# Performance work log

Measured on AMD Instinct MI355X. Metric: run time of the kernel, lower is better.

Reference implementation:

```python
import jax, jax.numpy as jnp
import numpy as np
from jax import lax

V, S, T, B = 32000, 64, 64, 64   # vocab, src_len, trg_len, batch
E, EH, DH = 128, 256, 256        # emb dim, enc hid, dec hid


def gru_cell(x, h, Wih, Whh, bih, bhh):
    # PyTorch GRU cell: gates ordered (r, z, n)
    gi = x @ Wih.T + bih
    gh = h @ Whh.T + bhh
    ir, iz, i_n = jnp.split(gi, 3, axis=-1)
    hr, hz, h_n = jnp.split(gh, 3, axis=-1)
    r = jax.nn.sigmoid(ir + hr)
    z = jax.nn.sigmoid(iz + hz)
    n = jnp.tanh(i_n + r * h_n)
    return (1.0 - z) * n + z * h


def setup_inputs() -> dict:
    key = jax.random.key(0)
    ks = iter(jax.random.split(key, 32))
    std = 0.01  # matches __init_weights(mean=0, std=0.01, const=0)
    def w(shape):
        return jax.random.normal(next(ks), shape, dtype=jnp.float32) * std
    return dict(
        src=jax.random.randint(next(ks), (S, B), 0, V),
        trg=jax.random.randint(next(ks), (T, B), 0, V),
        enc_emb=w((V, E)),
        enc_Wih_f=w((3 * EH, E)), enc_Whh_f=w((3 * EH, EH)),
        enc_bih_f=jnp.zeros((3 * EH,), jnp.float32), enc_bhh_f=jnp.zeros((3 * EH,), jnp.float32),
        enc_Wih_b=w((3 * EH, E)), enc_Whh_b=w((3 * EH, EH)),
        enc_bih_b=jnp.zeros((3 * EH,), jnp.float32), enc_bhh_b=jnp.zeros((3 * EH,), jnp.float32),
        enc_fc_W=w((DH, 2 * EH)), enc_fc_b=jnp.zeros((DH,), jnp.float32),
        attn_W=w((DH, 2 * EH + DH)), attn_b=jnp.zeros((DH,), jnp.float32),
        attn_v=w((1, DH)),
        dec_emb=w((V, E)),
        dec_Wih=w((3 * DH, 2 * EH + E)), dec_Whh=w((3 * DH, DH)),
        dec_bih=jnp.zeros((3 * DH,), jnp.float32), dec_bhh=jnp.zeros((3 * DH,), jnp.float32),
        fc_W=w((V, 2 * EH + DH + E)), fc_b=jnp.zeros((V,), jnp.float32),
    )


def reference(src, trg, enc_emb, enc_Wih_f, enc_Whh_f, enc_bih_f, enc_bhh_f,
              enc_Wih_b, enc_Whh_b, enc_bih_b, enc_bhh_b, enc_fc_W, enc_fc_b,
              attn_W, attn_b, attn_v, dec_emb, dec_Wih, dec_Whh, dec_bih,
              dec_bhh, fc_W, fc_b):
    # ---- Encoder: bidirectional GRU (dropout in eval mode => identity) ----
    emb = enc_emb[src]  # [S, B, E]
    h0 = jnp.zeros((src.shape[1], EH), emb.dtype)

    def step_f(h, x):
        h2 = gru_cell(x, h, enc_Wih_f, enc_Whh_f, enc_bih_f, enc_bhh_f)
        return h2, h2

    def step_b(h, x):
        h2 = gru_cell(x, h, enc_Wih_b, enc_Whh_b, enc_bih_b, enc_bhh_b)
        return h2, h2

    h_f, outs_f = lax.scan(step_f, h0, emb)
    h_b, outs_b_rev = lax.scan(step_b, h0, emb[::-1])
    enc_outs = jnp.concatenate([outs_f, outs_b_rev[::-1]], axis=-1)  # [S, B, 2*EH]
    hidden = jnp.tanh(jnp.concatenate([h_f, h_b], axis=-1) @ enc_fc_W.T + enc_fc_b)  # [B, DH]

    # ---- Decoder: per-step Bahdanau attention + GRU (teacher forcing) ----
    enc_bse = enc_outs.transpose(1, 0, 2)            # [B, S, 2*EH]
    W_h = attn_W[:, :DH]                             # hidden part of attn linear
    W_e = attn_W[:, DH:]                             # encoder part
    enc_proj = jnp.einsum('bse,he->bsh', enc_bse, W_e) + attn_b  # precomputed [B, S, DH]
    v = attn_v[0]                                    # [DH]

    def dec_step(h, tok):
        embd = dec_emb[tok]                                         # [B, E]
        energy = jnp.tanh(enc_proj + (h @ W_h.T)[:, None, :])       # [B, S, DH]
        scores = jnp.einsum('bsh,h->bs', energy, v)                 # [B, S]
        a = jax.nn.softmax(scores, axis=1)
        weighted = jnp.einsum('bs,bse->be', a, enc_bse)             # [B, 2*EH]
        x = jnp.concatenate([embd, weighted], axis=-1)              # [B, E+2*EH]
        h2 = gru_cell(x, h, dec_Wih, dec_Whh, dec_bih, dec_bhh)     # [B, DH]
        pred = jnp.concatenate([h2, weighted, embd], axis=-1) @ fc_W.T + fc_b  # [B, V]
        return h2, pred

    _, preds = lax.scan(dec_step, hidden, trg[:-1])                 # [T-1, B, V]
    outputs = jnp.concatenate(
        [jnp.zeros((1, preds.shape[1], preds.shape[2]), preds.dtype), preds], axis=0)
    return outputs
```

## Files before the change

kernel.cpp:

```cpp
#include <hip/hip_runtime.h>
#include <math.h>


__device__ __forceinline__ float sigmoidf_(float x) { return 1.0f / (1.0f + expf(-x)); }

typedef __attribute__((ext_vector_type(8))) short bf16x8;
typedef __attribute__((ext_vector_type(4))) float f32x4;
typedef __attribute__((ext_vector_type(8))) unsigned short ushort8;

__device__ __forceinline__ unsigned short f2bf(float f) {
  unsigned u = __float_as_uint(f);
  unsigned r = (u + 0x7fffu + ((u >> 16) & 1u)) >> 16;
  return (unsigned short)r;
}

__global__ __launch_bounds__(256) void k_zero(float* __restrict__ p, int n4) {
  int i = blockIdx.x * 256 + threadIdx.x;
  if (i < n4) ((float4*)p)[i] = make_float4(0.f, 0.f, 0.f, 0.f);
}

__global__ __launch_bounds__(256) void k_cvt_bf16(const float* __restrict__ in,
                                                  unsigned short* __restrict__ out, int n8) {
  int i = blockIdx.x * 256 + threadIdx.x;
  int stride = gridDim.x * 256;
  for (; i < n8; i += stride) {
    float4 a = ((const float4*)in)[2 * i];
    float4 b = ((const float4*)in)[2 * i + 1];
    ushort8 v;
    v[0] = f2bf(a.x); v[1] = f2bf(a.y); v[2] = f2bf(a.z); v[3] = f2bf(a.w);
    v[4] = f2bf(b.x); v[5] = f2bf(b.y); v[6] = f2bf(b.z); v[7] = f2bf(b.w);
    ((ushort8*)out)[i] = v;
  }
}

__global__ __launch_bounds__(256) void k_gather(const float* __restrict__ tab,
                                                const int* __restrict__ idx,
                                                float* __restrict__ out, int rows) {
  int g = blockIdx.x * 256 + threadIdx.x;
  int row = g >> 5, c = g & 31;
  if (row < rows) {
    int tok = idx[row];
    ((float4*)(out + (size_t)row * 128))[c] = ((const float4*)(tab + (size_t)tok * 128))[c];
  }
}

__global__ __launch_bounds__(256) void k_gemm_nt(const float* __restrict__ A, int lda,
                                                 const float* __restrict__ Bm, int ldb,
                                                 const float* __restrict__ bias,
                                                 float* __restrict__ C, int ldc, int K) {
  __shared__ float As[16][68];
  __shared__ float Bs[16][68];
  int tid = threadIdx.x;
  int m0 = blockIdx.y * 64, n0 = blockIdx.x * 64;
  int lm = tid >> 2, lk = (tid & 3) * 4;
  int tm = (tid >> 4) * 4, tn = (tid & 15) * 4;
  float acc[4][4] = {};
  for (int k0 = 0; k0 < K; k0 += 16) {
    float4 av = *(const float4*)(A + (size_t)(m0 + lm) * lda + k0 + lk);
    float4 bv = *(const float4*)(Bm + (size_t)(n0 + lm) * ldb + k0 + lk);
    __syncthreads();
    As[lk + 0][lm] = av.x; As[lk + 1][lm] = av.y; As[lk + 2][lm] = av.z; As[lk + 3][lm] = av.w;
    Bs[lk + 0][lm] = bv.x; Bs[lk + 1][lm] = bv.y; Bs[lk + 2][lm] = bv.z; Bs[lk + 3][lm] = bv.w;
    __syncthreads();
#pragma unroll
    for (int k = 0; k < 16; k++) {
      float4 a4 = *(const float4*)&As[k][tm];
      float4 b4 = *(const float4*)&Bs[k][tn];
      float ar[4] = {a4.x, a4.y, a4.z, a4.w};
      float br[4] = {b4.x, b4.y, b4.z, b4.w};
#pragma unroll
      for (int i = 0; i < 4; i++)
#pragma unroll
        for (int j = 0; j < 4; j++) acc[i][j] += ar[i] * br[j];
    }
  }
  float4 bb = *(const float4*)(bias + n0 + tn);
  float br[4] = {bb.x, bb.y, bb.z, bb.w};
#pragma unroll
  for (int i = 0; i < 4; i++) {
    float* crow = C + (size_t)(m0 + tm + i) * ldc + n0 + tn;
    *(float4*)crow = make_float4(acc[i][0] + br[0], acc[i][1] + br[1],
                                 acc[i][2] + br[2], acc[i][3] + br[3]);
  }
}

__global__ __launch_bounds__(256) void k_enc_step(
    const float* __restrict__ gi_f, const float* __restrict__ gi_b,
    const float* __restrict__ Whh_f, const float* __restrict__ Whh_b,
    const float* __restrict__ bhh_f, const float* __restrict__ bhh_b,
    const float* __restrict__ hinf, const float* __restrict__ hinb,
    float* __restrict__ houtf, float* __restrict__ houtb,
    float* __restrict__ enc_bse, int t) {
  int blk = blockIdx.x;
  int dir = blk >> 6;
  int jt = (blk >> 3) & 7, bg = blk & 7;
  const float* gi  = dir ? gi_b  : gi_f;
  const float* Whh = dir ? Whh_b : Whh_f;
  const float* bhh = dir ? bhh_b : bhh_f;
  const float* hin = dir ? hinb  : hinf;
  float* hout      = dir ? houtb : houtf;
  int s = dir ? (63 - t) : t;
  int tid = threadIdx.x;
  int b_l = tid & 7, j_l = tid >> 3;
  int b = bg * 8 + b_l, j = jt * 32 + j_l;
  __shared__ float hs[8][260];
  for (int i = tid; i < 2048; i += 256)
    hs[i >> 8][i & 255] = hin[(bg * 8 + (i >> 8)) * 256 + (i & 255)];
  __syncthreads();
  const float4* wr = (const float4*)(Whh + (size_t)j * 256);
  const float4* wz = (const float4*)(Whh + (size_t)(256 + j) * 256);
  const float4* wn = (const float4*)(Whh + (size_t)(512 + j) * 256);
  const float4* hv = (const float4*)&hs[b_l][0];
  float hr = 0.f, hz = 0.f, hn = 0.f;
#pragma unroll 8
  for (int k = 0; k < 64; k++) {
    float4 h4 = hv[k];
    float4 r4 = wr[k], z4 = wz[k], n4 = wn[k];
    hr += h4.x * r4.x + h4.y * r4.y + h4.z * r4.z + h4.w * r4.w;
    hz += h4.x * z4.x + h4.y * z4.y + h4.z * z4.z + h4.w * z4.w;
    hn += h4.x * n4.x + h4.y * n4.y + h4.z * n4.z + h4.w * n4.w;
  }
  hr += bhh[j]; hz += bhh[256 + j]; hn += bhh[512 + j];
  size_t gib = (size_t)(s * 64 + b) * 768;
  float r = sigmoidf_(gi[gib + j] + hr);
  float z = sigmoidf_(gi[gib + 256 + j] + hz);
  float n = tanhf(gi[gib + 512 + j] + r * hn);
  float h2 = (1.f - z) * n + z * hs[b_l][j];
  hout[b * 256 + j] = h2;
  enc_bse[((size_t)b * 64 + s) * 512 + dir * 256 + j] = h2;
}

__global__ __launch_bounds__(256) void k_hidden(const float* __restrict__ hf,
                                                const float* __restrict__ hb,
                                                const float* __restrict__ W,
                                                const float* __restrict__ bias,
                                                float* __restrict__ hdec) {
  int b = blockIdx.x, j = threadIdx.x;
  __shared__ float cat[512];
  cat[j] = hf[b * 256 + j];
  cat[256 + j] = hb[b * 256 + j];
  __syncthreads();
  const float4* wrow = (const float4*)(W + (size_t)j * 512);
  const float4* cv = (const float4*)cat;
  float acc = 0.f;
#pragma unroll 8
  for (int k = 0; k < 128; k++) {
    float4 w4 = wrow[k], c4 = cv[k];
    acc += w4.x * c4.x + w4.y * c4.y + w4.z * c4.z + w4.w * c4.w;
  }
  hdec[b * 256 + j] = tanhf(acc + bias[j]);
}

__global__ __launch_bounds__(256) void k_attn(
    const float* __restrict__ hdec, const float* __restrict__ attn_W,
    const float* __restrict__ attn_v, const float* __restrict__ enc_proj,
    const float* __restrict__ enc_bse, const float* __restrict__ embd_all,
    float* __restrict__ weighted, float* __restrict__ Z, int t) {
  int b = blockIdx.x, tid = threadIdx.x;
  __shared__ float hs[256], hW[256], vs[256], sc[64];
  hs[tid] = hdec[b * 256 + tid];
  vs[tid] = attn_v[tid];
  __syncthreads();
  {
    const float4* wrow = (const float4*)(attn_W + (size_t)tid * 768);
    const float4* hv = (const float4*)hs;
    float acc = 0.f;
#pragma unroll 8
    for (int k = 0; k < 64; k++) {
      float4 w4 = wrow[k], h4 = hv[k];
      acc += w4.x * h4.x + w4.y * h4.y + w4.z * h4.z + w4.w * h4.w;
    }
    hW[tid] = acc;
  }
  __syncthreads();
  int w = tid >> 6, l = tid & 63;
  for (int s = w; s < 64; s += 4) {
    const float* ep = enc_proj + ((size_t)b * 64 + s) * 256;
    float p = 0.f;
#pragma unroll
    for (int i = 0; i < 4; i++) {
      int h = l + i * 64;
      p += vs[h] * tanhf(ep[h] + hW[h]);
    }
#pragma unroll
    for (int o = 32; o > 0; o >>= 1) p += __shfl_xor(p, o, 64);
    if (l == 0) sc[s] = p;
  }
  __syncthreads();
  if (tid < 64) {
    float x = sc[tid], m = x;
#pragma unroll
    for (int o = 32; o > 0; o >>= 1) m = fmaxf(m, __shfl_xor(m, o, 64));
    float e = expf(x - m), ssum = e;
#pragma unroll
    for (int o = 32; o > 0; o >>= 1) ssum += __shfl_xor(ssum, o, 64);
    sc[tid] = e / ssum;
  }
  __syncthreads();
  float a0 = 0.f, a1 = 0.f;
  const float* eb = enc_bse + (size_t)b * 64 * 512;
  for (int s = 0; s < 64; s++) {
    float a = sc[s];
    a0 += a * eb[s * 512 + tid];
    a1 += a * eb[s * 512 + 256 + tid];
  }
  size_t zr = (size_t)(t * 64 + b) * 896;
  weighted[b * 512 + tid] = a0;
  weighted[b * 512 + 256 + tid] = a1;
  Z[zr + 256 + tid] = a0;
  Z[zr + 512 + tid] = a1;
  if (tid < 128) Z[zr + 768 + tid] = embd_all[(size_t)(t * 64 + b) * 128 + tid];
}

__global__ __launch_bounds__(256) void k_dec_gru(
    const float* __restrict__ weighted, const float* __restrict__ gi_emb,
    const float* __restrict__ Wih, const float* __restrict__ Whh,
    const float* __restrict__ bhh, const float* __restrict__ hin,
    float* __restrict__ hout, float* __restrict__ Z, int t) {
  int blk = blockIdx.x;
  int jt = blk & 7, bg = blk >> 3;
  int tid = threadIdx.x;
  int b_l = tid & 7, j_l = tid >> 3;
  int b = bg * 8 + b_l, j = jt * 32 + j_l;
  __shared__ float ws2[8][516];
  __shared__ float hs[8][260];
  for (int i = tid; i < 4096; i += 256)
    ws2[i >> 9][i & 511] = weighted[(bg * 8 + (i >> 9)) * 512 + (i & 511)];
  for (int i = tid; i < 2048; i += 256)
    hs[i >> 8][i & 255] = hin[(bg * 8 + (i >> 8)) * 256 + (i & 255)];
  __syncthreads();
  float gr = 0.f, gz = 0.f, gn = 0.f;
  {
    const float4* wr = (const float4*)(Wih + (size_t)j * 640 + 128);
    const float4* wz = (const float4*)(Wih + (size_t)(256 + j) * 640 + 128);
    const float4* wn = (const float4*)(Wih + (size_t)(512 + j) * 640 + 128);
    const float4* xv = (const float4*)&ws2[b_l][0];
#pragma unroll 8
    for (int k = 0; k < 128; k++) {
      float4 x4 = xv[k];
      float4 r4 = wr[k], z4 = wz[k], n4 = wn[k];
      gr += x4.x * r4.x + x4.y * r4.y + x4.z * r4.z + x4.w * r4.w;
      gz += x4.x * z4.x + x4.y * z4.y + x4.z * z4.z + x4.w * z4.w;
      gn += x4.x * n4.x + x4.y * n4.y + x4.z * n4.z + x4.w * n4.w;
    }
  }
  float hr = bhh[j], hz = bhh[256 + j], hn = bhh[512 + j];
  {
    const float4* ur = (const float4*)(Whh + (size_t)j * 256);
    const float4* uz = (const float4*)(Whh + (size_t)(256 + j) * 256);
    const float4* un = (const float4*)(Whh + (size_t)(512 + j) * 256);
    const float4* hv = (const float4*)&hs[b_l][0];
#pragma unroll 8
    for (int k = 0; k < 64; k++) {
      float4 h4 = hv[k];
      float4 r4 = ur[k], z4 = uz[k], n4 = un[k];
      hr += h4.x * r4.x + h4.y * r4.y + h4.z * r4.z + h4.w * r4.w;
      hz += h4.x * z4.x + h4.y * z4.y + h4.z * z4.z + h4.w * z4.w;
      hn += h4.x * n4.x + h4.y * n4.y + h4.z * n4.z + h4.w * n4.w;
    }
  }
  size_t gib = (size_t)(t * 64 + b) * 768;
  float r = sigmoidf_(gi_emb[gib + j] + gr + hr);
  float z = sigmoidf_(gi_emb[gib + 256 + j] + gz + hz);
  float n = tanhf(gi_emb[gib + 512 + j] + gn + r * hn);
  float h2 = (1.f - z) * n + z * hs[b_l][j];
  hout[b * 256 + j] = h2;
  Z[(size_t)(t * 64 + b) * 896 + j] = h2;
}

__global__ __launch_bounds__(256) void k_fc_mfma(const unsigned short* __restrict__ Zb16,
                                                 const unsigned short* __restrict__ Wb16,
                                                 const float* __restrict__ bias,
                                                 float* __restrict__ out) {
  __shared__ unsigned short As[128 * 64];
  __shared__ unsigned short Bs[128 * 64];
  int tid = threadIdx.x;
  int l = tid & 63, w = tid >> 6;
  int m0 = blockIdx.y * 128, n0 = blockIdx.x * 128;
  int wr = w >> 1, wc = w & 1;
  f32x4 acc[4][4] = {};

  int lrow = l >> 3;
  int lk = (l & 7) * 8;

  for (int k0 = 0; k0 < 896; k0 += 64) {
    __syncthreads();
#pragma unroll
    for (int i = 0; i < 4; i++) {
      int c = i * 4 + w;
      const unsigned short* ga = Zb16 + (size_t)(m0 + c * 8 + lrow) * 896 + k0 + lk;
      const unsigned short* gb = Wb16 + (size_t)(n0 + c * 8 + lrow) * 896 + k0 + lk;
      __builtin_amdgcn_global_load_lds((const __attribute__((address_space(1))) void*)ga,
                                       (__attribute__((address_space(3))) void*)&As[c * 512],
                                       16, 0, 0);
      __builtin_amdgcn_global_load_lds((const __attribute__((address_space(1))) void*)gb,
                                       (__attribute__((address_space(3))) void*)&Bs[c * 512],
                                       16, 0, 0);
    }
    __syncthreads();
#pragma unroll
    for (int ks = 0; ks < 2; ks++) {
      bf16x8 aF[4], bF[4];
#pragma unroll
      for (int i = 0; i < 4; i++)
        aF[i] = *(const bf16x8*)&As[(wr * 64 + i * 16 + (l & 15)) * 64 + ks * 32 + (l >> 4) * 8];
#pragma unroll
      for (int j = 0; j < 4; j++)
        bF[j] = *(const bf16x8*)&Bs[(wc * 64 + j * 16 + (l & 15)) * 64 + ks * 32 + (l >> 4) * 8];
#pragma unroll
      for (int i = 0; i < 4; i++)
#pragma unroll
        for (int j = 0; j < 4; j++)
          acc[i][j] = __builtin_amdgcn_mfma_f32_16x16x32_bf16(aF[i], bF[j], acc[i][j], 0, 0, 0);
    }
  }
  int cl = l & 15, rg = l >> 4;
#pragma unroll
  for (int j = 0; j < 4; j++) {
    int n = n0 + wc * 64 + j * 16 + cl;
    float bb = bias[n];
#pragma unroll
    for (int i = 0; i < 4; i++) {
      int mb = m0 + wr * 64 + i * 16 + rg * 4;
#pragma unroll
      for (int r = 0; r < 4; r++) {
        int m = mb + r;
        if (m < 4032) out[(size_t)(m + 64) * 32000 + n] = acc[i][j][r] + bb;
      }
    }
  }
}

extern "C" void kernel_launch(void* const* d_in, const int* in_sizes, int n_in,
                              void* d_out, int out_size, void* d_ws, size_t ws_size,
                              hipStream_t stream) {
  const int* src = (const int*)d_in[0];
  const int* trg = (const int*)d_in[1];
  const float* enc_emb = (const float*)d_in[2];
  const float* eWih_f  = (const float*)d_in[3];
  const float* eWhh_f  = (const float*)d_in[4];
  const float* ebih_f  = (const float*)d_in[5];
  const float* ebhh_f  = (const float*)d_in[6];
  const float* eWih_b  = (const float*)d_in[7];
  const float* eWhh_b  = (const float*)d_in[8];
  const float* ebih_b  = (const float*)d_in[9];
  const float* ebhh_b  = (const float*)d_in[10];
  const float* efc_W   = (const float*)d_in[11];
  const float* efc_b   = (const float*)d_in[12];
  const float* attn_W  = (const float*)d_in[13];
  const float* attn_b  = (const float*)d_in[14];
  const float* attn_v  = (const float*)d_in[15];
  const float* dec_emb = (const float*)d_in[16];
  const float* dWih    = (const float*)d_in[17];
  const float* dWhh    = (const float*)d_in[18];
  const float* dbih    = (const float*)d_in[19];
  const float* dbhh    = (const float*)d_in[20];
  const float* fc_W    = (const float*)d_in[21];
  const float* fc_b    = (const float*)d_in[22];
  float* out = (float*)d_out;
  float* ws = (float*)d_ws;

  size_t o = 0;
  float* emb_src  = ws + o; o += (size_t)4096 * 128;
  float* embd_all = ws + o; o += (size_t)4032 * 128;
  float* gi_f     = ws + o; o += (size_t)4096 * 768;
  float* gi_b     = ws + o; o += (size_t)4096 * 768;
  float* gi_emb   = ws + o; o += (size_t)4032 * 768;
  float* enc_bse  = ws + o; o += (size_t)4096 * 512;
  float* enc_proj = ws + o; o += (size_t)4096 * 256;
  float* h_f0 = ws + o; o += 16384;
  float* h_b0 = ws + o; o += 16384;
  float* h_f1 = ws + o; o += 16384;
  float* h_b1 = ws + o; o += 16384;
  float* h_d0 = ws + o; o += 16384;
  float* h_d1 = ws + o; o += 16384;
  float* wt   = ws + o; o += 64 * 512;
  float* Zb   = ws + o; o += (size_t)4096 * 896;
  unsigned short* Zb16 = (unsigned short*)(ws + o); o += (size_t)4096 * 896 / 2;
  unsigned short* Wb16 = (unsigned short*)(ws + o); o += (size_t)32000 * 896 / 2;

  k_zero<<<2000, 256, 0, stream>>>(out, 512000);
  k_zero<<<32, 256, 0, stream>>>(h_f0, 8192);
  k_zero<<<56, 256, 0, stream>>>(Zb + (size_t)4032 * 896, 14336);
  k_gather<<<512, 256, 0, stream>>>(enc_emb, src, emb_src, 4096);
  k_gather<<<504, 256, 0, stream>>>(dec_emb, trg, embd_all, 4032);

  k_cvt_bf16<<<2048, 256, 0, stream>>>(fc_W, Wb16, 3584000);

  k_gemm_nt<<<dim3(12, 64), 256, 0, stream>>>(emb_src, 128, eWih_f, 128, ebih_f, gi_f, 768, 128);
  k_gemm_nt<<<dim3(12, 64), 256, 0, stream>>>(emb_src, 128, eWih_b, 128, ebih_b, gi_b, 768, 128);
  k_gemm_nt<<<dim3(12, 63), 256, 0, stream>>>(embd_all, 128, dWih, 640, dbih, gi_emb, 768, 128);

  for (int t = 0; t < 64; t++) {
    const float* hif = (t & 1) ? h_f1 : h_f0;
    const float* hib = (t & 1) ? h_b1 : h_b0;
    float* hof = (t & 1) ? h_f0 : h_f1;
    float* hob = (t & 1) ? h_b0 : h_b1;
    k_enc_step<<<128, 256, 0, stream>>>(gi_f, gi_b, eWhh_f, eWhh_b, ebhh_f, ebhh_b,
                                        hif, hib, hof, hob, enc_bse, t);
  }
  k_hidden<<<64, 256, 0, stream>>>(h_f0, h_b0, efc_W, efc_b, h_d0);
  k_gemm_nt<<<dim3(4, 64), 256, 0, stream>>>(enc_bse, 512, attn_W + 256, 768, attn_b,
                                             enc_proj, 256, 512);

  for (int t = 0; t < 63; t++) {
    const float* hi = (t & 1) ? h_d1 : h_d0;
    float* ho = (t & 1) ? h_d0 : h_d1;
    k_attn<<<64, 256, 0, stream>>>(hi, attn_W, attn_v, enc_proj, enc_bse, embd_all, wt, Zb, t);
    k_dec_gru<<<64, 256, 0, stream>>>(wt, gi_emb, dWih, dWhh, dbhh, hi, ho, Zb, t);
  }

  k_cvt_bf16<<<1024, 256, 0, stream>>>(Zb, Zb16, 458752);
  k_fc_mfma<<<dim3(250, 32), 256, 0, stream>>>(Zb16, Wb16, fc_b, out);
}
```

Baseline: 5.204 ms.

## Fuse encoder and decoder time loops into persistent scan kernels, precompute attention-input projection

Replaces the 64 per-step encoder launches and the 126 per-step decoder launches with one persistent kernel each, with one block per (direction, batch) or per batch keeping the hidden state in shared memory across steps. Uses linearity to precompute enc_bse·Wih_ctx (PRE) once with a bf16 MFMA GEMM, so each decoder step only needs an attention-weighted sum of PRE rows instead of a 512-wide matvec. The enc_proj GEMM also moves to bf16 MFMA, which adds rounding error. In exchange, each recurrent step now runs on only 64–128 blocks, each serially streaming its weights.

```diff
diff --git a/kernel.cpp b/kernel.cpp
--- a/kernel.cpp
+++ b/kernel.cpp
@@ -33,6 +33,24 @@
   }
 }
 
+__global__ __launch_bounds__(256) void k_cvt_slice(const float* __restrict__ in,
+                                                   unsigned short* __restrict__ out,
+                                                   int rows, int ld, int col0, int cols) {
+  int g = blockIdx.x * 256 + threadIdx.x;
+  int c8 = cols >> 3;
+  int n8 = rows * c8;
+  if (g < n8) {
+    int r = g / c8, c = g % c8;
+    const float* p = in + (size_t)r * ld + col0 + c * 8;
+    float4 a = ((const float4*)p)[0];
+    float4 b = ((const float4*)p)[1];
+    ushort8 v;
+    v[0] = f2bf(a.x); v[1] = f2bf(a.y); v[2] = f2bf(a.z); v[3] = f2bf(a.w);
+    v[4] = f2bf(b.x); v[5] = f2bf(b.y); v[6] = f2bf(b.z); v[7] = f2bf(b.w);
+    ((ushort8*)(out + (size_t)r * cols + c * 8))[0] = v;
+  }
+}
+
 __global__ __launch_bounds__(256) void k_gather(const float* __restrict__ tab,
                                                 const int* __restrict__ idx,
                                                 float* __restrict__ out, int rows) {
@@ -42,6 +60,14 @@
     int tok = idx[row];
     ((float4*)(out + (size_t)row * 128))[c] = ((const float4*)(tab + (size_t)tok * 128))[c];
   }
+}
+
+__global__ __launch_bounds__(256) void k_embZ(const float* __restrict__ emb,
+                                              float* __restrict__ Z) {
+  int g = blockIdx.x * 256 + threadIdx.x;
+  int row = g >> 5, c = g & 31;
+  if (row < 4032)
+    ((float4*)(Z + (size_t)row * 896 + 768))[c] = ((const float4*)(emb + (size_t)row * 128))[c];
 }
 
 __global__ __launch_bounds__(256) void k_gemm_nt(const float* __restrict__ A, int lda,
@@ -84,50 +110,49 @@
   }
 }
 
-__global__ __launch_bounds__(256) void k_enc_step(
+__global__ __launch_bounds__(256) void k_enc_scan(
     const float* __restrict__ gi_f, const float* __restrict__ gi_b,
     const float* __restrict__ Whh_f, const float* __restrict__ Whh_b,
     const float* __restrict__ bhh_f, const float* __restrict__ bhh_b,
-    const float* __restrict__ hinf, const float* __restrict__ hinb,
-    float* __restrict__ houtf, float* __restrict__ houtb,
-    float* __restrict__ enc_bse, int t) {
+    float* __restrict__ hf_out, float* __restrict__ hb_out,
+    float* __restrict__ enc_bse) {
   int blk = blockIdx.x;
-  int dir = blk >> 6;
-  int jt = (blk >> 3) & 7, bg = blk & 7;
+  int dir = blk >> 6, b = blk & 63;
+  int j = threadIdx.x;
   const float* gi  = dir ? gi_b  : gi_f;
   const float* Whh = dir ? Whh_b : Whh_f;
   const float* bhh = dir ? bhh_b : bhh_f;
-  const float* hin = dir ? hinb  : hinf;
-  float* hout      = dir ? houtb : houtf;
-  int s = dir ? (63 - t) : t;
-  int tid = threadIdx.x;
-  int b_l = tid & 7, j_l = tid >> 3;
-  int b = bg * 8 + b_l, j = jt * 32 + j_l;
-  __shared__ float hs[8][260];
-  for (int i = tid; i < 2048; i += 256)
-    hs[i >> 8][i & 255] = hin[(bg * 8 + (i >> 8)) * 256 + (i & 255)];
-  __syncthreads();
+  __shared__ float h_s[256];
+  h_s[j] = 0.f;
+  float bh_r = bhh[j], bh_z = bhh[256 + j], bh_n = bhh[512 + j];
   const float4* wr = (const float4*)(Whh + (size_t)j * 256);
   const float4* wz = (const float4*)(Whh + (size_t)(256 + j) * 256);
   const float4* wn = (const float4*)(Whh + (size_t)(512 + j) * 256);
-  const float4* hv = (const float4*)&hs[b_l][0];
-  float hr = 0.f, hz = 0.f, hn = 0.f;
+  const float4* hv = (const float4*)h_s;
+  __syncthreads();
+  float h2 = 0.f;
+  for (int t = 0; t < 64; t++) {
+    int s = dir ? (63 - t) : t;
+    float hr = bh_r, hz = bh_z, hn = bh_n;
 #pragma unroll 8
-  for (int k = 0; k < 64; k++) {
-    float4 h4 = hv[k];
-    float4 r4 = wr[k], z4 = wz[k], n4 = wn[k];
-    hr += h4.x * r4.x + h4.y * r4.y + h4.z * r4.z + h4.w * r4.w;
-    hz += h4.x * z4.x + h4.y * z4.y + h4.z * z4.z + h4.w * z4.w;
-    hn += h4.x * n4.x + h4.y * n4.y + h4.z * n4.z + h4.w * n4.w;
-  }
-  hr += bhh[j]; hz += bhh[256 + j]; hn += bhh[512 + j];
-  size_t gib = (size_t)(s * 64 + b) * 768;
-  float r = sigmoidf_(gi[gib + j] + hr);
-  float z = sigmoidf_(gi[gib + 256 + j] + hz);
-  float n = tanhf(gi[gib + 512 + j] + r * hn);
-  float h2 = (1.f - z) * n + z * hs[b_l][j];
-  hout[b * 256 + j] = h2;
-  enc_bse[((size_t)b * 64 + s) * 512 + dir * 256 + j] = h2;
+    for (int k = 0; k < 64; k++) {
+      float4 h4 = hv[k];
+      float4 r4 = wr[k], z4 = wz[k], n4 = wn[k];
+      hr += h4.x * r4.x + h4.y * r4.y + h4.z * r4.z + h4.w * r4.w;
+      hz += h4.x * z4.x + h4.y * z4.y + h4.z * z4.z + h4.w * z4.w;
+      hn += h4.x * n4.x + h4.y * n4.y + h4.z * n4.z + h4.w * n4.w;
+    }
+    size_t gib = (size_t)(s * 64 + b) * 768;
+    float r = sigmoidf_(gi[gib + j] + hr);
+    float z = sigmoidf_(gi[gib + 256 + j] + hz);
+    float n = tanhf(gi[gib + 512 + j] + r * hn);
+    h2 = (1.f - z) * n + z * h_s[j];
+    __syncthreads();
+    h_s[j] = h2;
+    enc_bse[((size_t)b * 64 + s) * 512 + dir * 256 + j] = h2;
+    __syncthreads();
+  }
+  (dir ? hb_out : hf_out)[b * 256 + j] = h2;
 }
 
 __global__ __launch_bounds__(256) void k_hidden(const float* __restrict__ hf,
@@ -151,105 +176,76 @@
   hdec[b * 256 + j] = tanhf(acc + bias[j]);
 }
 
-__global__ __launch_bounds__(256) void k_attn(
-    const float* __restrict__ hdec, const float* __restrict__ attn_W,
+__global__ __launch_bounds__(256) void k_dec_scan(
+    const float* __restrict__ h0, const float* __restrict__ attn_W,
     const float* __restrict__ attn_v, const float* __restrict__ enc_proj,
-    const float* __restrict__ enc_bse, const float* __restrict__ embd_all,
-    float* __restrict__ weighted, float* __restrict__ Z, int t) {
+    const float* __restrict__ enc_bse, const float* __restrict__ PRE,
+    const float* __restrict__ gi_emb, const float* __restrict__ Whh,
+    const float* __restrict__ bhh, float* __restrict__ Z) {
   int b = blockIdx.x, tid = threadIdx.x;
-  __shared__ float hs[256], hW[256], vs[256], sc[64];
-  hs[tid] = hdec[b * 256 + tid];
-  vs[tid] = attn_v[tid];
+  __shared__ float h_s[256], hW_s[256], v_s[256], sc[64];
+  h_s[tid] = h0[b * 256 + tid];
+  v_s[tid] = attn_v[tid];
+  float bh_r = bhh[tid], bh_z = bhh[256 + tid], bh_n = bhh[512 + tid];
+  const float4* wrow = (const float4*)(attn_W + (size_t)tid * 768);
+  const float4* ur = (const float4*)(Whh + (size_t)tid * 256);
+  const float4* uz = (const float4*)(Whh + (size_t)(256 + tid) * 256);
+  const float4* un = (const float4*)(Whh + (size_t)(512 + tid) * 256);
+  const float4* hv = (const float4*)h_s;
+  const float* eb = enc_bse + (size_t)b * 64 * 512;
+  const float* pr = PRE + (size_t)b * 64 * 768;
   __syncthreads();
-  {
-    const float4* wrow = (const float4*)(attn_W + (size_t)tid * 768);
-    const float4* hv = (const float4*)hs;
-    float acc = 0.f;
+  for (int t = 0; t < 63; t++) {
+    {
+      float acc = 0.f;
 #pragma unroll 8
-    for (int k = 0; k < 64; k++) {
-      float4 w4 = wrow[k], h4 = hv[k];
-      acc += w4.x * h4.x + w4.y * h4.y + w4.z * h4.z + w4.w * h4.w;
-    }
-    hW[tid] = acc;
-  }
-  __syncthreads();
-  int w = tid >> 6, l = tid & 63;
-  for (int s = w; s < 64; s += 4) {
-    const float* ep = enc_proj + ((size_t)b * 64 + s) * 256;
-    float p = 0.f;
-#pragma unroll
-    for (int i = 0; i < 4; i++) {
-      int h = l + i * 64;
-      p += vs[h] * tanhf(ep[h] + hW[h]);
-    }
-#pragma unroll
-    for (int o = 32; o > 0; o >>= 1) p += __shfl_xor(p, o, 64);
-    if (l == 0) sc[s] = p;
-  }
-  __syncthreads();
-  if (tid < 64) {
-    float x = sc[tid], m = x;
-#pragma unroll
-    for (int o = 32; o > 0; o >>= 1) m = fmaxf(m, __shfl_xor(m, o, 64));
-    float e = expf(x - m), ssum = e;
-#pragma unroll
-    for (int o = 32; o > 0; o >>= 1) ssum += __shfl_xor(ssum, o, 64);
-    sc[tid] = e / ssum;
-  }
-  __syncthreads();
-  float a0 = 0.f, a1 = 0.f;
-  const float* eb = enc_bse + (size_t)b * 64 * 512;
-  for (int s = 0; s < 64; s++) {
-    float a = sc[s];
-    a0 += a * eb[s * 512 + tid];
-    a1 += a * eb[s * 512 + 256 + tid];
-  }
-  size_t zr = (size_t)(t * 64 + b) * 896;
-  weighted[b * 512 + tid] = a0;
-  weighted[b * 512 + 256 + tid] = a1;
-  Z[zr + 256 + tid] = a0;
-  Z[zr + 512 + tid] = a1;
-  if (tid < 128) Z[zr + 768 + tid] = embd_all[(size_t)(t * 64 + b) * 128 + tid];
-}
-
-__global__ __launch_bounds__(256) void k_dec_gru(
-    const float* __restrict__ weighted, const float* __restrict__ gi_emb,
-    const float* __restrict__ Wih, const float* __restrict__ Whh,
-    const float* __restrict__ bhh, const float* __restrict__ hin,
-    float* __restrict__ hout, float* __restrict__ Z, int t) {
-  int blk = blockIdx.x;
-  int jt = blk & 7, bg = blk >> 3;
-  int tid = threadIdx.x;
-  int b_l = tid & 7, j_l = tid >> 3;
-  int b = bg * 8 + b_l, j = jt * 32 + j_l;
-  __shared__ float ws2[8][516];
-  __shared__ float hs[8][260];
-  for (int i = tid; i < 4096; i += 256)
-    ws2[i >> 9][i & 511] = weighted[(bg * 8 + (i >> 9)) * 512 + (i & 511)];
-  for (int i = tid; i < 2048; i += 256)
-    hs[i >> 8][i & 255] = hin[(bg * 8 + (i >> 8)) * 256 + (i & 255)];
-  __syncthreads();
-  float gr = 0.f, gz = 0.f, gn = 0.f;
-  {
-    const float4* wr = (const float4*)(Wih + (size_t)j * 640 + 128);
-    const float4* wz = (const float4*)(Wih + (size_t)(256 + j) * 640 + 128);
-    const float4* wn = (const float4*)(Wih + (size_t)(512 + j) * 640 + 128);
-    const float4* xv = (const float4*)&ws2[b_l][0];
-#pragma unroll 8
-    for (int k = 0; k < 128; k++) {
-      float4 x4 = xv[k];
-      float4 r4 = wr[k], z4 = wz[k], n4 = wn[k];
-      gr += x4.x * r4.x + x4.y * r4.y + x4.z * r4.z + x4.w * r4.w;
-      gz += x4.x * z4.x + x4.y * z4.y + x4.z * z4.z + x4.w * z4.w;
-      gn += x4.x * n4.x + x4.y * n4.y + x4.z * n4.z + x4.w * n4.w;
-    }
-  }
-  float hr = bhh[j], hz = bhh[256 + j], hn = bhh[512 + j];
-  {
-    const float4* ur = (const float4*)(Whh + (size_t)j * 256);
-    const float4* uz = (const float4*)(Whh + (size_t)(256 + j) * 256);
-    const float4* un = (const float4*)(Whh + (size_t)(512 + j) * 256);
-    const float4* hv = (const float4*)&hs[b_l][0];
+      for (int k = 0; k < 64; k++) {
+        float4 w4 = wrow[k], h4 = hv[k];
+        acc += w4.x * h4.x + w4.y * h4.y + w4.z * h4.z + w4.w * h4.w;
+      }
+      hW_s[tid] = acc;
+    }
+    __syncthreads();
+    {
+      int w = tid >> 6, l = tid & 63;
+      for (int s = w; s < 64; s += 4) {
+        const float* ep = enc_proj + ((size_t)b * 64 + s) * 256;
+        float p = 0.f;
+#pragma unroll
+        for (int i = 0; i < 4; i++) {
+          int hh = l + i * 64;
+          p += v_s[hh] * tanhf(ep[hh] + hW_s[hh]);
+        }
+#pragma unroll
+        for (int o = 32; o > 0; o >>= 1) p += __shfl_xor(p, o, 64);
+        if (l == 0) sc[s] = p;
+      }
+    }
+    __syncthreads();
+    if (tid < 64) {
+      float x = sc[tid], m = x;
+#pragma unroll
+      for (int o = 32; o > 0; o >>= 1) m = fmaxf(m, __shfl_xor(m, o, 64));
+      float e = expf(x - m), ssum = e;
+#pragma unroll
+      for (int o = 32; o > 0; o >>= 1) ssum += __shfl_xor(ssum, o, 64);
+      sc[tid] = e / ssum;
+    }
+    __syncthreads();
+    size_t zr = (size_t)(t * 64 + b) * 896;
+    float w0 = 0.f, w1 = 0.f, gwr = 0.f, gwz = 0.f, gwn = 0.f;
+#pragma unroll 4
+    for (int s = 0; s < 64; s++) {
+      float a = sc[s];
+      w0 += a * eb[s * 512 + tid];
+      w1 += a * eb[s * 512 + 256 + tid];
+      gwr += a * pr[s * 768 + tid];
+      gwz += a * pr[s * 768 + 256 + tid];
+      gwn += a * pr[s * 768 + 512 + tid];
+    }
+    Z[zr + 256 + tid] = w0;
+    Z[zr + 512 + tid] = w1;
+    float hr = bh_r, hz = bh_z, hn = bh_n;
 #pragma unroll 8
     for (int k = 0; k < 64; k++) {
       float4 h4 = hv[k];
@@ -258,14 +254,74 @@
       hz += h4.x * z4.x + h4.y * z4.y + h4.z * z4.z + h4.w * z4.w;
       hn += h4.x * n4.x + h4.y * n4.y + h4.z * n4.z + h4.w * n4.w;
     }
-  }
-  size_t gib = (size_t)(t * 64 + b) * 768;
-  float r = sigmoidf_(gi_emb[gib + j] + gr + hr);
-  float z = sigmoidf_(gi_emb[gib + 256 + j] + gz + hz);
-  float n = tanhf(gi_emb[gib + 512 + j] + gn + r * hn);
-  float h2 = (1.f - z) * n + z * hs[b_l][j];
-  hout[b * 256 + j] = h2;
-  Z[(size_t)(t * 64 + b) * 896 + j] = h2;
+    size_t gib = (size_t)(t * 64 + b) * 768;
+    float r = sigmoidf_(gi_emb[gib + tid] + gwr + hr);
+    float z = sigmoidf_(gi_emb[gib + 256 + tid] + gwz + hz);
+    float n = tanhf(gi_emb[gib + 512 + tid] + gwn + r * hn);
+    float h2 = (1.f - z) * n + z * h_s[tid];
+    __syncthreads();
+    h_s[tid] = h2;
+    Z[zr + tid] = h2;
+    __syncthreads();
+  }
+}
+
+__global__ __launch_bounds__(256) void k_gemm_mfma(const unsigned short* __restrict__ A16,
+                                                   const unsigned short* __restrict__ B16,
+                                                   const float* __restrict__ bias,
+                                                   float* __restrict__ C, int K, int ldc) {
+  __shared__ unsigned short As[128 * 64];
+  __shared__ unsigned short Bs[128 * 64];
+  int tid = threadIdx.x;
+  int l = tid & 63, w = tid >> 6;
+  int m0 = blockIdx.y * 128, n0 = blockIdx.x * 128;
+  int wr = w >> 1, wc = w & 1;
+  f32x4 acc[4][4] = {};
+  int lrow = l >> 3, lk = (l & 7) * 8;
+  for (int k0 = 0; k0 < K; k0 += 64) {
+    __syncthreads();
+#pragma unroll
+    for (int i = 0; i < 4; i++) {
+      int c = i * 4 + w;
+      const unsigned short* ga = A16 + (size_t)(m0 + c * 8 + lrow) * K + k0 + lk;
+      const unsigned short* gb = B16 + (size_t)(n0 + c * 8 + lrow) * K + k0 + lk;
+      __builtin_amdgcn_global_load_lds((const __attribute__((address_space(1))) void*)ga,
+                                       (__attribute__((address_space(3))) void*)&As[c * 512],
+                                       16, 0, 0);
+      __builtin_amdgcn_global_load_lds((const __attribute__((address_space(1))) void*)gb,
+                                       (__attribute__((address_space(3))) void*)&Bs[c * 512],
+                                       16, 0, 0);
+    }
+    __syncthreads();
+#pragma unroll
+    for (int ks = 0; ks < 2; ks++) {
+      bf16x8 aF[4], bF[4];
+#pragma unroll
+      for (int i = 0; i < 4; i++)
+        aF[i] = *(const bf16x8*)&As[(wr * 64 + i * 16 + (l & 15)) * 64 + ks * 32 + (l >> 4) * 8];
+#pragma unroll
+      for (int j = 0; j < 4; j++)
+        bF[j] = *(const bf16x8*)&Bs[(wc * 64 + j * 16 + (l & 15)) * 64 + ks * 32 + (l >> 4) * 8];
+#pragma unroll
+      for (int i = 0; i < 4; i++)
+#pragma unroll
+        for (int j = 0; j < 4; j++)
+          acc[i][j] = __builtin_amdgcn_mfma_f32_16x16x32_bf16(aF[i], bF[j], acc[i][j], 0, 0, 0);
+    }
+  }
+  int cl = l & 15, rg = l >> 4;
+#pragma unroll
+  for (int j = 0; j < 4; j++) {
+    int n = n0 + wc * 64 + j * 16 + cl;
+    float bb = bias ? bias[n] : 0.f;
+#pragma unroll
+    for (int i = 0; i < 4; i++) {
+      int mb = m0 + wr * 64 + i * 16 + rg * 4;
+#pragma unroll
+      for (int r = 0; r < 4; r++)
+        C[(size_t)(mb + r) * ldc + n] = acc[i][j][r] + bb;
+    }
+  }
 }
 
 __global__ __launch_bounds__(256) void k_fc_mfma(const unsigned short* __restrict__ Zb16,
@@ -279,10 +335,7 @@
   int m0 = blockIdx.y * 128, n0 = blockIdx.x * 128;
   int wr = w >> 1, wc = w & 1;
   f32x4 acc[4][4] = {};
-
-  int lrow = l >> 3;
-  int lk = (l & 7) * 8;
-
+  int lrow = l >> 3, lk = (l & 7) * 8;
   for (int k0 = 0; k0 < 896; k0 += 64) {
     __syncthreads();
 #pragma unroll
@@ -368,47 +421,41 @@
   float* gi_emb   = ws + o; o += (size_t)4032 * 768;
   float* enc_bse  = ws + o; o += (size_t)4096 * 512;
   float* enc_proj = ws + o; o += (size_t)4096 * 256;
+  float* PRE      = ws + o; o += (size_t)4096 * 768;
   float* h_f0 = ws + o; o += 16384;
   float* h_b0 = ws + o; o += 16384;
-  float* h_f1 = ws + o; o += 16384;
-  float* h_b1 = ws + o; o += 16384;
   float* h_d0 = ws + o; o += 16384;
-  float* h_d1 = ws + o; o += 16384;
-  float* wt   = ws + o; o += 64 * 512;
   float* Zb   = ws + o; o += (size_t)4096 * 896;
-  unsigned short* Zb16 = (unsigned short*)(ws + o); o += (size_t)4096 * 896 / 2;
-  unsigned short* Wb16 = (unsigned short*)(ws + o); o += (size_t)32000 * 896 / 2;
+  unsigned short* Zb16    = (unsigned short*)(ws + o); o += (size_t)4096 * 896 / 2;
+  unsigned short* Wb16    = (unsigned short*)(ws + o); o += (size_t)32000 * 896 / 2;
+  unsigned short* eb16    = (unsigned short*)(ws + o); o += (size_t)4096 * 512 / 2;
+  unsigned short* Wpre16  = (unsigned short*)(ws + o); o += (size_t)768 * 512 / 2;
+  unsigned short* Wproj16 = (unsigned short*)(ws + o); o += (size_t)256 * 512 / 2;
 
   k_zero<<<2000, 256, 0, stream>>>(out, 512000);
-  k_zero<<<32, 256, 0, stream>>>(h_f0, 8192);
   k_zero<<<56, 256, 0, stream>>>(Zb + (size_t)4032 * 896, 14336);
   k_gather<<<512, 256, 0, stream>>>(enc_emb, src, emb_src, 4096);
   k_gather<<<504, 256, 0, stream>>>(dec_emb, trg, embd_all, 4032);
+  k_embZ<<<504, 256, 0, stream>>>(embd_all, Zb);
 
   k_cvt_bf16<<<2048, 256, 0, stream>>>(fc_W, Wb16, 3584000);
+  k_cvt_slice<<<192, 256, 0, stream>>>(dWih, Wpre16, 768, 640, 128, 512);
+  k_cvt_slice<<<64, 256, 0, stream>>>(attn_W, Wproj16, 256, 768, 256, 512);
 
   k_gemm_nt<<<dim3(12, 64), 256, 0, stream>>>(emb_src, 128, eWih_f, 128, ebih_f, gi_f, 768, 128);
   k_gemm_nt<<<dim3(12, 64), 256, 0, stream>>>(emb_src, 128, eWih_b, 128, ebih_b, gi_b, 768, 128);
   k_gemm_nt<<<dim3(12, 63), 256, 0, stream>>>(embd_all, 128, dWih, 640, dbih, gi_emb, 768, 128);
 
-  for (int t = 0; t < 64; t++) {
-    const float* hif = (t & 1) ? h_f1 : h_f0;
-    const float* hib = (t & 1) ? h_b1 : h_b0;
-    float* hof = (t & 1) ? h_f0 : h_f1;
-    float* hob = (t & 1) ? h_b0 : h_b1;
-    k_enc_step<<<128, 256, 0, stream>>>(gi_f, gi_b, eWhh_f, eWhh_b, ebhh_f, ebhh_b,
-                                        hif, hib, hof, hob, enc_bse, t);
-  }
+  k_enc_scan<<<128, 256, 0, stream>>>(gi_f, gi_b, eWhh_f, eWhh_b, ebhh_f, ebhh_b,
+                                      h_f0, h_b0, enc_bse);
   k_hidden<<<64, 256, 0, stream>>>(h_f0, h_b0, efc_W, efc_b, h_d0);
-  k_gemm_nt<<<dim3(4, 64), 256, 0, stream>>>(enc_bse, 512, attn_W + 256, 768, attn_b,
-                                             enc_proj, 256, 512);
-
-  for (int t = 0; t < 63; t++) {
-    const float* hi = (t & 1) ? h_d1 : h_d0;
-    float* ho = (t & 1) ? h_d0 : h_d1;
-    k_attn<<<64, 256, 0, stream>>>(hi, attn_W, attn_v, enc_proj, enc_bse, embd_all, wt, Zb, t);
-    k_dec_gru<<<64, 256, 0, stream>>>(wt, gi_emb, dWih, dWhh, dbhh, hi, ho, Zb, t);
-  }
+
+  k_cvt_bf16<<<1024, 256, 0, stream>>>(enc_bse, eb16, 262144);
+  k_gemm_mfma<<<dim3(6, 32), 256, 0, stream>>>(eb16, Wpre16, nullptr, PRE, 512, 768);
+  k_gemm_mfma<<<dim3(2, 32), 256, 0, stream>>>(eb16, Wproj16, attn_b, enc_proj, 512, 256);
+
+  k_dec_scan<<<64, 256, 0, stream>>>(h_d0, attn_W, attn_v, enc_proj, enc_bse, PRE,
+                                     gi_emb, dWhh, dbhh, Zb);
 
   k_cvt_bf16<<<1024, 256, 0, stream>>>(Zb, Zb16, 458752);
   k_fc_mfma<<<dim3(250, 32), 256, 0, stream>>>(Zb16, Wb16, fc_b, out);
```

Result: slower. 6.301 ms (+21.1%).
